# Performance work log

Measured on AMD Instinct MI355X. Metric: run time of the kernel, lower is better.

## Reference

```python
import jax, jax.numpy as jnp
import numpy as np

FILTER_SIZE = 4
STRIDE = 1
DELTA = FILTER_SIZE - STRIDE  # extra wrap-around columns from PbcTensor


def setup_inputs() -> dict:
    key = jax.random.key(0)
    kx, kw, kb = jax.random.split(key, 3)
    B, C_in, C_out, L = 64, 8, 8, 65536
    x = jax.random.normal(kx, (B, C_in, L), dtype=jnp.float32)
    # Conv1d weight (out_channel, in_channel, filter_size) and bias, torch-style init scale
    fan_in = C_in * FILTER_SIZE
    bound = 1.0 / np.sqrt(fan_in)
    W = jax.random.uniform(kw, (C_out, C_in, FILTER_SIZE), dtype=jnp.float32, minval=-bound, maxval=bound)
    b = jax.random.uniform(kb, (C_out,), dtype=jnp.float32, minval=-bound, maxval=bound)
    return {"x": x, "W": W, "b": b}


def reference(x, W, b):
    # tensordot(x, PbcTensor) with the almost-identity (L, L+del) matrix is
    # exactly circular padding: append the first `del` columns to the end.
    xp = jnp.concatenate([x, x[:, :, :DELTA]], axis=-1)  # (B, C_in, L+del)
    # Conv1d, stride 1, VALID padding -> output length L
    out = jax.lax.conv_general_dilated(
        xp, W,
        window_strides=(STRIDE,),
        padding='VALID',
        dimension_numbers=('NCH', 'OIH', 'NCH'),
    )
    return out + b[None, :, None]
```

## Files before the change

### kernel.cpp

```cpp
#include <hip/hip_runtime.h>

#define BATCH 64
#define CIN 8
#define COUT 8
#define LEN 65536
#define FS 4
#define TILE 1024

__global__ __launch_bounds__(256, 4) void conv_pbc_kernel(
    const float* __restrict__ x,
    const float* __restrict__ W,
    const float* __restrict__ bias,
    float* __restrict__ out)
{
    __shared__ float sW[COUT * CIN * FS];
    __shared__ float sB[COUT];

    const int tid = threadIdx.x;
    if (tid < COUT * CIN * FS) sW[tid] = W[tid];
    if (tid < COUT)            sB[tid] = bias[tid];
    __syncthreads();

    const int blocksPerBatch = LEN / TILE;
    const int b    = blockIdx.x / blocksPerBatch;
    const int tile = blockIdx.x % blocksPerBatch;
    const int l0   = tile * TILE + tid * 4;

    const float* xb = x + (size_t)b * CIN * LEN;

    float acc[COUT][4];
#pragma unroll
    for (int co = 0; co < COUT; ++co) {
        const float bb = sB[co];
        acc[co][0] = bb; acc[co][1] = bb; acc[co][2] = bb; acc[co][3] = bb;
    }

    const bool fast = (l0 + 8 <= LEN);

#pragma unroll 2
    for (int ci = 0; ci < CIN; ++ci) {
        const float* xc = xb + (size_t)ci * LEN;
        float xv[8];
        if (fast) {
            const float4 v0 = *reinterpret_cast<const float4*>(xc + l0);
            const float4 v1 = *reinterpret_cast<const float4*>(xc + l0 + 4);
            xv[0] = v0.x; xv[1] = v0.y; xv[2] = v0.z; xv[3] = v0.w;
            xv[4] = v1.x; xv[5] = v1.y; xv[6] = v1.z; xv[7] = v1.w;
        } else {
#pragma unroll
            for (int j = 0; j < 8; ++j)
                xv[j] = xc[(l0 + j) & (LEN - 1)];
        }

#pragma unroll
        for (int co = 0; co < COUT; ++co) {
#pragma unroll
            for (int k = 0; k < FS; ++k) {
                const float w = sW[(co * CIN + ci) * FS + k];
#pragma unroll
                for (int p = 0; p < 4; ++p)
                    acc[co][p] += w * xv[p + k];
            }
        }
    }

    float* ob = out + (size_t)b * COUT * LEN + l0;
#pragma unroll
    for (int co = 0; co < COUT; ++co) {
        float4 v;
        v.x = acc[co][0]; v.y = acc[co][1]; v.z = acc[co][2]; v.w = acc[co][3];
        *reinterpret_cast<float4*>(ob + (size_t)co * LEN) = v;
    }
}

extern "C" void kernel_launch(void* const* d_in, const int* in_sizes, int n_in,
                              void* d_out, int out_size, void* d_ws, size_t ws_size,
                              hipStream_t stream) {
    const float* x    = (const float*)d_in[0];
    const float* W    = (const float*)d_in[1];
    const float* bias = (const float*)d_in[2];
    float* out = (float*)d_out;

    const int blocksPerBatch = LEN / TILE;
    const dim3 grid(BATCH * blocksPerBatch);
    const dim3 block(256);
    conv_pbc_kernel<<<grid, block, 0, stream>>>(x, W, bias, out);
}
```

Before: 50.24 us.

## Stage input tile in shared memory with halo and use nontemporal stores

Each block now loads its 8-channel x tile once into LDS with all eight channel loads issued up front, plus a small wrap-around halo, instead of each thread doing two overlapping global float4 loads per channel. The channel loop is fully unrolled and reads from LDS. Output stores become nontemporal. This cuts redundant global traffic and raises memory-level parallelism, at the cost of extra LDS use and a barrier.

Measured after the change: 50.41 us. About the same (+0.3%).

```diff
diff --git a/kernel.cpp b/kernel.cpp
--- a/kernel.cpp
+++ b/kernel.cpp
@@ -6,6 +6,9 @@
 #define LEN 65536
 #define FS 4
 #define TILE 1024
+#define PADL (TILE + 8)
+
+typedef float floatx4 __attribute__((ext_vector_type(4)));
 
 __global__ __launch_bounds__(256, 4) void conv_pbc_kernel(
     const float* __restrict__ x,
@@ -13,20 +16,38 @@
     const float* __restrict__ bias,
     float* __restrict__ out)
 {
+    __shared__ float sX[CIN][PADL];
     __shared__ float sW[COUT * CIN * FS];
     __shared__ float sB[COUT];
 
     const int tid = threadIdx.x;
     if (tid < COUT * CIN * FS) sW[tid] = W[tid];
     if (tid < COUT)            sB[tid] = bias[tid];
-    __syncthreads();
 
     const int blocksPerBatch = LEN / TILE;
     const int b    = blockIdx.x / blocksPerBatch;
     const int tile = blockIdx.x % blocksPerBatch;
-    const int l0   = tile * TILE + tid * 4;
+    const int base = tile * TILE;
 
     const float* xb = x + (size_t)b * CIN * LEN;
+
+    floatx4 r[CIN];
+#pragma unroll
+    for (int ci = 0; ci < CIN; ++ci)
+        r[ci] = *reinterpret_cast<const floatx4*>(xb + (size_t)ci * LEN + base + tid * 4);
+#pragma unroll
+    for (int ci = 0; ci < CIN; ++ci)
+        *reinterpret_cast<floatx4*>(&sX[ci][tid * 4]) = r[ci];
+
+    if (tid < CIN) {
+        const int hbase = (base + TILE) & (LEN - 1);
+        const floatx4 h = *reinterpret_cast<const floatx4*>(xb + (size_t)tid * LEN + hbase);
+        sX[tid][TILE + 0] = h.x;
+        sX[tid][TILE + 1] = h.y;
+        sX[tid][TILE + 2] = h.z;
+        sX[tid][TILE + 3] = h.w;
+    }
+    __syncthreads();
 
     float acc[COUT][4];
 #pragma unroll
@@ -35,22 +56,11 @@
         acc[co][0] = bb; acc[co][1] = bb; acc[co][2] = bb; acc[co][3] = bb;
     }
 
-    const bool fast = (l0 + 8 <= LEN);
-
-#pragma unroll 2
+#pragma unroll
     for (int ci = 0; ci < CIN; ++ci) {
-        const float* xc = xb + (size_t)ci * LEN;
-        float xv[8];
-        if (fast) {
-            const float4 v0 = *reinterpret_cast<const float4*>(xc + l0);
-            const float4 v1 = *reinterpret_cast<const float4*>(xc + l0 + 4);
-            xv[0] = v0.x; xv[1] = v0.y; xv[2] = v0.z; xv[3] = v0.w;
-            xv[4] = v1.x; xv[5] = v1.y; xv[6] = v1.z; xv[7] = v1.w;
-        } else {
-#pragma unroll
-            for (int j = 0; j < 8; ++j)
-                xv[j] = xc[(l0 + j) & (LEN - 1)];
-        }
+        const floatx4 a = *reinterpret_cast<const floatx4*>(&sX[ci][tid * 4]);
+        const floatx4 q = *reinterpret_cast<const floatx4*>(&sX[ci][tid * 4 + 4]);
+        const float xv[8] = {a.x, a.y, a.z, a.w, q.x, q.y, q.z, q.w};
 
 #pragma unroll
         for (int co = 0; co < COUT; ++co) {
@@ -64,12 +74,12 @@
         }
     }
 
-    float* ob = out + (size_t)b * COUT * LEN + l0;
+    float* ob = out + (size_t)b * COUT * LEN + base + tid * 4;
 #pragma unroll
     for (int co = 0; co < COUT; ++co) {
-        float4 v;
+        floatx4 v;
         v.x = acc[co][0]; v.y = acc[co][1]; v.z = acc[co][2]; v.w = acc[co][3];
-        *reinterpret_cast<float4*>(ob + (size_t)co * LEN) = v;
+        __builtin_nontemporal_store(v, reinterpret_cast<floatx4*>(ob + (size_t)co * LEN));
     }
 }
 
```
